# Performance work log

Hardware: AMD Instinct MI355X
Metric: run time of the kernel (lower is better)

Reference implementation:

```python
import jax, jax.numpy as jnp
import numpy as np

N_EMBD = 1024
N_HEAD = 16

def setup_inputs() -> dict:
    key = jax.random.key(0)
    ks = jax.random.split(key, 5)
    B, T, C = 4, 2048, N_EMBD
    x = jax.random.normal(ks[0], (B, T, C), dtype=jnp.float32)
    # torch nn.Linear weights: [out_features, in_features]
    w_attn = jax.random.normal(ks[1], (3 * C, C), dtype=jnp.float32) * (1.0 / np.sqrt(C))
    b_attn = jax.random.normal(ks[2], (3 * C,), dtype=jnp.float32) * 0.02
    w_proj = jax.random.normal(ks[3], (C, C), dtype=jnp.float32) * (1.0 / np.sqrt(C))
    b_proj = jax.random.normal(ks[4], (C,), dtype=jnp.float32) * 0.02
    return {"x": x, "w_attn": w_attn, "b_attn": b_attn, "w_proj": w_proj, "b_proj": b_proj}

def reference(x, w_attn, b_attn, w_proj, b_proj):
    B, T, C = x.shape
    H = N_HEAD
    D = C // H
    qkv = jnp.einsum('btc,oc->bto', x, w_attn) + b_attn  # [B,T,3C]
    q, k, v = jnp.split(qkv, 3, axis=-1)
    # [B,H,T,D]
    q = q.reshape(B, T, H, D).transpose(0, 2, 1, 3)
    k = k.reshape(B, T, H, D).transpose(0, 2, 1, 3)
    v = v.reshape(B, T, H, D).transpose(0, 2, 1, 3)
    att = jnp.einsum('bhqd,bhkd->bhqk', q, k) * (1.0 / np.sqrt(D))
    causal = jnp.tril(jnp.ones((T, T), dtype=bool))
    att = jnp.where(causal[None, None], att, -jnp.inf)
    att = jax.nn.softmax(att, axis=-1)
    y = jnp.einsum('bhqk,bhkd->bhqd', att, v)
    y = y.transpose(0, 2, 1, 3).reshape(B, T, C)
    return jnp.einsum('btc,oc->bto', y, w_proj) + b_proj
```

## Files before the change

kernel.cpp:

```cpp
#include <hip/hip_runtime.h>
#include <hip/hip_bf16.h>
#include <math.h>
#include <stdint.h>


typedef __attribute__((ext_vector_type(8))) short bf16x8;
typedef __attribute__((ext_vector_type(4))) float f32x4;

#define MFMA16(a, b, c) __builtin_amdgcn_mfma_f32_16x16x32_bf16((a), (b), (c), 0, 0, 0)

#define GLOAD_LDS16(gptr, lptr)                                                        \
  __builtin_amdgcn_global_load_lds((const __attribute__((address_space(1))) void*)(gptr), \
                                   (__attribute__((address_space(3))) void*)(lptr), 16, 0, 0)

__device__ __forceinline__ short f2bf(float f) {
  uint32_t u = __builtin_bit_cast(uint32_t, f);
  u = (u + 0x7FFFu + ((u >> 16) & 1u)) >> 16;
  return (short)u;
}

__device__ __forceinline__ uint32_t cvtpk_bf16(float a, float b) {
  uint32_t pk;
  asm("v_cvt_pk_bf16_f32 %0, %1, %2" : "=v"(pk) : "v"(a), "v"(b));
  return pk;
}

__global__ void cvt3_f32_bf16(const float* __restrict__ x, short* __restrict__ ox, int nx4,
                              const float* __restrict__ wa, short* __restrict__ owa, int nwa4,
                              const float* __restrict__ wp, short* __restrict__ owp, int nwp4) {
  int i = blockIdx.x * 256 + threadIdx.x;
  const float* src;
  short* dst;
  int j;
  if (i < nx4) {
    src = x; dst = ox; j = i;
  } else if (i < nx4 + nwa4) {
    src = wa; dst = owa; j = i - nx4;
  } else if (i < nx4 + nwa4 + nwp4) {
    src = wp; dst = owp; j = i - nx4 - nwa4;
  } else {
    return;
  }
  float4 v = ((const float4*)src)[j];
  short4 o;
  o.x = f2bf(v.x); o.y = f2bf(v.y); o.z = f2bf(v.z); o.w = f2bf(v.w);
  ((short4*)dst)[j] = o;
}

template <int MODE>
__global__ __launch_bounds__(256, 3)
void gemm_bt(const short* __restrict__ A, const short* __restrict__ B,
             const float* __restrict__ bias, int K, int N,
             short* __restrict__ q, short* __restrict__ kk,
             short* __restrict__ vt, float* __restrict__ out) {
  __shared__ short As[128 * 32];
  __shared__ short Bs[128 * 32];
  const int tid = threadIdx.x;
  const int lane = tid & 63;
  const int w = tid >> 6;
  const int wm = w >> 1, wn = w & 1;
  const int bn = blockIdx.x, bm = blockIdx.y;
  const char* Ab = (const char*)A + (size_t)bm * 128 * K * 2;
  const char* Bb = (const char*)B + (size_t)bn * 128 * K * 2;
  const int rstride = K * 2;

  f32x4 acc[4][4] = {};

  for (int k0 = 0; k0 < K; k0 += 32) {
#pragma unroll
    for (int i = 0; i < 2; ++i) {
      const int off = i * 4096 + w * 1024 + lane * 16;
      const int row = off >> 6, cb = off & 63;
      GLOAD_LDS16(Ab + (size_t)row * rstride + k0 * 2 + cb, (char*)As + off);
      GLOAD_LDS16(Bb + (size_t)row * rstride + k0 * 2 + cb, (char*)Bs + off);
    }
    __syncthreads();

    bf16x8 a[4], b[4];
#pragma unroll
    for (int mi = 0; mi < 4; ++mi)
      a[mi] = *(const bf16x8*)&As[(wm * 64 + mi * 16 + (lane & 15)) * 32 + (lane >> 4) * 8];
#pragma unroll
    for (int ni = 0; ni < 4; ++ni)
      b[ni] = *(const bf16x8*)&Bs[(wn * 64 + ni * 16 + (lane & 15)) * 32 + (lane >> 4) * 8];
#pragma unroll
    for (int mi = 0; mi < 4; ++mi)
#pragma unroll
      for (int ni = 0; ni < 4; ++ni)
        acc[mi][ni] = MFMA16(a[mi], b[ni], acc[mi][ni]);
    __syncthreads();
  }

  if (MODE == 0) {
    const int part = bn >> 3;
    if (part == 2) {
      const int bb = bm >> 4;
#pragma unroll
      for (int mi = 0; mi < 4; ++mi) {
        const int t0 = (bm & 15) * 128 + wm * 64 + mi * 16 + (lane >> 4) * 4;
#pragma unroll
        for (int ni = 0; ni < 4; ++ni) {
          const int c = bn * 128 + wn * 64 + ni * 16 + (lane & 15) - 2048;
          const int h = c >> 6, d = c & 63;
          const float bv = bias[c + 2048];
          uint2 pk;
          pk.x = cvtpk_bf16(acc[mi][ni][0] + bv, acc[mi][ni][1] + bv);
          pk.y = cvtpk_bf16(acc[mi][ni][2] + bv, acc[mi][ni][3] + bv);
          *(uint2*)&vt[(((size_t)bb * 16 + h) * 64 + d) * 2048 + t0] = pk;
        }
      }
    } else {
      short* dst = (part == 0) ? q : kk;
      const float sc = (part == 0) ? 0.125f * 1.44269504f : 1.0f;
#pragma unroll
      for (int mi = 0; mi < 4; ++mi) {
#pragma unroll
        for (int ni = 0; ni < 4; ++ni) {
          const int n = bn * 128 + wn * 64 + ni * 16 + (lane & 15);
          const int c = n & 1023, h = c >> 6, d = c & 63;
          const float bv = bias[n];
#pragma unroll
          for (int r = 0; r < 4; ++r) {
            const int m = bm * 128 + wm * 64 + mi * 16 + (lane >> 4) * 4 + r;
            const int bb = m >> 11, t = m & 2047;
            dst[(((size_t)bb * 16 + h) * 2048 + t) * 64 + d] =
                f2bf((acc[mi][ni][r] + bv) * sc);
          }
        }
      }
    }
  } else {
#pragma unroll
    for (int mi = 0; mi < 4; ++mi)
#pragma unroll
      for (int ni = 0; ni < 4; ++ni) {
        const int n = bn * 128 + wn * 64 + ni * 16 + (lane & 15);
        const float bv = bias[n];
#pragma unroll
        for (int r = 0; r < 4; ++r) {
          const int m = bm * 128 + wm * 64 + mi * 16 + (lane >> 4) * 4 + r;
          out[(size_t)m * N + n] = acc[mi][ni][r] + bv;
        }
      }
  }
}

__global__ __launch_bounds__(256, 3)
void attn64(const short* __restrict__ Q, const short* __restrict__ Kd,
            const short* __restrict__ Vt, short* __restrict__ Y) {
  const int o = blockIdx.x;
  const int swz = (o & 7) * 256 + (o >> 3);
  const int bh = swz >> 5;
  const int qb = 31 - (swz & 31);
  const int tid = threadIdx.x, lane = tid & 63, w = tid >> 6;

  __shared__ short Ks[2][64 * 64];
  __shared__ short Vs[2][64 * 64];
  __shared__ short Ps[4][16 * 64];

  const char* qg = (const char*)(Q + (size_t)bh * 2048 * 64);
  const char* kg = (const char*)(Kd + (size_t)bh * 2048 * 64);
  const char* vg = (const char*)(Vt + (size_t)bh * 64 * 2048);

  bf16x8 qa[2];
  const int qrowA = qb * 64 + w * 16 + (lane & 15);
#pragma unroll
  for (int dc = 0; dc < 2; ++dc)
    qa[dc] = *(const bf16x8*)(qg + (size_t)qrowA * 128 + dc * 64 + (lane >> 4) * 16);

  bf16x8 bones;
  {
    const short v = ((lane & 15) == 0) ? (short)0x3F80 : (short)0;
#pragma unroll
    for (int j = 0; j < 8; ++j) bones[j] = v;
  }

  auto stage = [&](int buf, int kt) {
#pragma unroll
    for (int i = 0; i < 2; ++i) {
      const int off = i * 4096 + w * 1024 + lane * 16;
      const int row = off >> 7, cb = off & 127;
      const int scb = cb ^ ((row & 7) << 4);
      GLOAD_LDS16(kg + (size_t)(kt * 64 + row) * 128 + scb, (char*)Ks[buf] + off);
      GLOAD_LDS16(vg + (size_t)row * 4096 + kt * 128 + scb, (char*)Vs[buf] + off);
    }
  };

  f32x4 oacc[4] = {};
  f32x4 lacc = {};
  const int qrowD = qb * 64 + w * 16 + (lane >> 4) * 4;

  stage(0, 0);
  __syncthreads();
  int cur = 0;

  for (int kt = 0; kt <= qb; ++kt) {
    if (kt < qb) stage(cur ^ 1, kt + 1);

    const char* ks = (const char*)Ks[cur];
    const char* vs = (const char*)Vs[cur];

    f32x4 sacc[4] = {};
    __builtin_amdgcn_s_setprio(1);
#pragma unroll
    for (int dc = 0; dc < 2; ++dc) {
#pragma unroll
      for (int ni = 0; ni < 4; ++ni) {
        const int row = ni * 16 + (lane & 15);
        const int bo = (dc * 64 + (lane >> 4) * 16) ^ ((row & 7) << 4);
        bf16x8 kf = *(const bf16x8*)(ks + row * 128 + bo);
        sacc[ni] = MFMA16(qa[dc], kf, sacc[ni]);
      }
    }
    __builtin_amdgcn_s_setprio(0);

    if (kt == qb) {
#pragma unroll
      for (int ni = 0; ni < 4; ++ni) {
        const int col = kt * 64 + ni * 16 + (lane & 15);
#pragma unroll
        for (int r = 0; r < 4; ++r)
          if (col > qrowD + r) sacc[ni][r] = -INFINITY;
      }
    }

#pragma unroll
    for (int r = 0; r < 4; ++r)
#pragma unroll
      for (int ni = 0; ni < 4; ++ni)
        sacc[ni][r] = exp2f(sacc[ni][r]);

    char* pw = (char*)&Ps[w][0];
#pragma unroll
    for (int r = 0; r < 4; ++r) {
      const int prow = (lane >> 4) * 4 + r;
      const int rowoff = prow * 128;
      const int sw = (prow & 7) << 4;
#pragma unroll
      for (int ni = 0; ni < 4; ni += 2) {
        const uint32_t pk = cvtpk_bf16(sacc[ni][r], sacc[ni + 1][r]);
        const int a0 = rowoff + ((((ni) * 16 + (lane & 15)) * 2) ^ sw);
        const int a1 = rowoff + ((((ni + 1) * 16 + (lane & 15)) * 2) ^ sw);
        *(short*)(pw + a0) = (short)(pk & 0xFFFFu);
        *(short*)(pw + a1) = (short)(pk >> 16);
      }
    }
    asm volatile("s_waitcnt lgkmcnt(0)" ::: "memory");

    bf16x8 pa[2];
#pragma unroll
    for (int kc = 0; kc < 2; ++kc) {
      const int prow = lane & 15;
      const int pbo = (kc * 64 + (lane >> 4) * 16) ^ ((prow & 7) << 4);
      pa[kc] = *(const bf16x8*)(pw + prow * 128 + pbo);
    }

    __builtin_amdgcn_s_setprio(1);
#pragma unroll
    for (int nd = 0; nd < 4; ++nd)
#pragma unroll
      for (int kc = 0; kc < 2; ++kc) {
        const int row = nd * 16 + (lane & 15);
        const int bo = (kc * 64 + (lane >> 4) * 16) ^ ((row & 7) << 4);
        bf16x8 vf = *(const bf16x8*)(vs + row * 128 + bo);
        oacc[nd] = MFMA16(pa[kc], vf, oacc[nd]);
      }
    lacc = MFMA16(pa[0], bones, lacc);
    lacc = MFMA16(pa[1], bones, lacc);
    __builtin_amdgcn_s_setprio(0);

    __syncthreads();
    cur ^= 1;
  }

  float linv[4];
#pragma unroll
  for (int r = 0; r < 4; ++r) {
    const float l = __shfl(lacc[r], lane & 48);
    linv[r] = 1.0f / l;
  }

  char* pw = (char*)&Ps[w][0];
  const int qloc0 = (lane >> 4) * 4;
#pragma unroll
  for (int nd = 0; nd < 4; ++nd)
#pragma unroll
    for (int r = 0; r < 4; ++r) {
      const int row = qloc0 + r;
      const int bo = (nd * 32 + (lane & 15) * 2) ^ ((row & 7) << 4);
      *(short*)(pw + row * 128 + bo) = f2bf(oacc[nd][r] * linv[r]);
    }
  asm volatile("s_waitcnt lgkmcnt(0)" ::: "memory");

  const int b = bh >> 4, h = bh & 15;
#pragma unroll
  for (int half = 0; half < 2; ++half) {
    const int qlocal = half * 8 + (lane >> 3);
    const int dstart = (lane & 7) * 8;
    const int bo = (dstart * 2) ^ ((qlocal & 7) << 4);
    bf16x8 v = *(const bf16x8*)(pw + qlocal * 128 + bo);
    const int t = qb * 64 + w * 16 + qlocal;
    *(bf16x8*)&Y[((size_t)b * 2048 + t) * 1024 + h * 64 + dstart] = v;
  }
}

extern "C" void kernel_launch(void* const* d_in, const int* in_sizes, int n_in,
                              void* d_out, int out_size, void* d_ws, size_t ws_size,
                              hipStream_t stream) {
  const float* x = (const float*)d_in[0];
  const float* w_attn = (const float*)d_in[1];
  const float* b_attn = (const float*)d_in[2];
  const float* w_proj = (const float*)d_in[3];
  const float* b_proj = (const float*)d_in[4];
  float* out = (float*)d_out;

  char* ws = (char*)d_ws;
  size_t o = 0;
  const size_t SZ = (size_t)8192 * 1024 * 2;
  short* xb = (short*)(ws + o);  o += SZ;
  short* wab = (short*)(ws + o); o += (size_t)3072 * 1024 * 2;
  short* wpb = (short*)(ws + o); o += (size_t)1024 * 1024 * 2;
  short* qw = (short*)(ws + o);  o += SZ;
  short* kw = (short*)(ws + o);  o += SZ;
  short* vtw = (short*)(ws + o); o += SZ;
  short* yb = xb;

  cvt3_f32_bf16<<<12288, 256, 0, stream>>>(x, xb, 2097152,
                                           w_attn, wab, 786432,
                                           w_proj, wpb, 262144);

  gemm_bt<0><<<dim3(24, 64), 256, 0, stream>>>(xb, wab, b_attn, 1024, 3072,
                                               qw, kw, vtw, nullptr);
  attn64<<<2048, 256, 0, stream>>>(qw, kw, vtw, yb);
  gemm_bt<1><<<dim3(8, 64), 256, 0, stream>>>(yb, wpb, b_proj, 1024, 1024,
                                              nullptr, nullptr, nullptr, out);
}
```

Measured before the change: 282.0 us.

## Process two 64-row query sub-tiles per attention block to reuse K/V tiles

Each attention block now handles 128 query rows as two 64-row sub-tiles. It loads each K/V tile into LDS once and uses it for both sub-tiles, and the grid is halved to 1024 blocks. This is meant to halve K/V global loads and staging per query row and to amortise barriers. It raises register pressure because Q fragments and accumulators are doubled, it makes the causal workload per block coarser, and launch bounds are changed to target 4 blocks per CU.

```diff
diff --git a/kernel.cpp b/kernel.cpp
--- a/kernel.cpp
+++ b/kernel.cpp
@@ -145,13 +145,13 @@
   }
 }
 
-__global__ __launch_bounds__(256, 3)
+__global__ __launch_bounds__(256, 4)
 void attn64(const short* __restrict__ Q, const short* __restrict__ Kd,
             const short* __restrict__ Vt, short* __restrict__ Y) {
   const int o = blockIdx.x;
-  const int swz = (o & 7) * 256 + (o >> 3);
-  const int bh = swz >> 5;
-  const int qb = 31 - (swz & 31);
+  const int swz = (o & 7) * 128 + (o >> 3);
+  const int bh = swz >> 4;
+  const int qb = 15 - (swz & 15);
   const int tid = threadIdx.x, lane = tid & 63, w = tid >> 6;
 
   __shared__ short Ks[2][64 * 64];
@@ -162,11 +162,14 @@
   const char* kg = (const char*)(Kd + (size_t)bh * 2048 * 64);
   const char* vg = (const char*)(Vt + (size_t)bh * 64 * 2048);
 
-  bf16x8 qa[2];
-  const int qrowA = qb * 64 + w * 16 + (lane & 15);
-#pragma unroll
-  for (int dc = 0; dc < 2; ++dc)
-    qa[dc] = *(const bf16x8*)(qg + (size_t)qrowA * 128 + dc * 64 + (lane >> 4) * 16);
+  bf16x8 qa[2][2];
+#pragma unroll
+  for (int s = 0; s < 2; ++s) {
+    const int qrowA = qb * 128 + s * 64 + w * 16 + (lane & 15);
+#pragma unroll
+    for (int dc = 0; dc < 2; ++dc)
+      qa[s][dc] = *(const bf16x8*)(qg + (size_t)qrowA * 128 + dc * 64 + (lane >> 4) * 16);
+  }
 
   bf16x8 bones;
   {
@@ -186,121 +189,130 @@
     }
   };
 
-  f32x4 oacc[4] = {};
-  f32x4 lacc = {};
-  const int qrowD = qb * 64 + w * 16 + (lane >> 4) * 4;
+  f32x4 oacc[2][4] = {};
+  f32x4 lacc[2] = {};
+  const int ktmax = 2 * qb + 1;
 
   stage(0, 0);
   __syncthreads();
   int cur = 0;
 
-  for (int kt = 0; kt <= qb; ++kt) {
-    if (kt < qb) stage(cur ^ 1, kt + 1);
+  for (int kt = 0; kt <= ktmax; ++kt) {
+    if (kt < ktmax) stage(cur ^ 1, kt + 1);
 
     const char* ks = (const char*)Ks[cur];
     const char* vs = (const char*)Vs[cur];
-
-    f32x4 sacc[4] = {};
-    __builtin_amdgcn_s_setprio(1);
-#pragma unroll
-    for (int dc = 0; dc < 2; ++dc) {
-#pragma unroll
-      for (int ni = 0; ni < 4; ++ni) {
-        const int row = ni * 16 + (lane & 15);
-        const int bo = (dc * 64 + (lane >> 4) * 16) ^ ((row & 7) << 4);
-        bf16x8 kf = *(const bf16x8*)(ks + row * 128 + bo);
-        sacc[ni] = MFMA16(qa[dc], kf, sacc[ni]);
-      }
-    }
-    __builtin_amdgcn_s_setprio(0);
-
-    if (kt == qb) {
-#pragma unroll
-      for (int ni = 0; ni < 4; ++ni) {
-        const int col = kt * 64 + ni * 16 + (lane & 15);
-#pragma unroll
-        for (int r = 0; r < 4; ++r)
-          if (col > qrowD + r) sacc[ni][r] = -INFINITY;
-      }
-    }
-
-#pragma unroll
-    for (int r = 0; r < 4; ++r)
-#pragma unroll
-      for (int ni = 0; ni < 4; ++ni)
-        sacc[ni][r] = exp2f(sacc[ni][r]);
-
     char* pw = (char*)&Ps[w][0];
-#pragma unroll
-    for (int r = 0; r < 4; ++r) {
-      const int prow = (lane >> 4) * 4 + r;
-      const int rowoff = prow * 128;
-      const int sw = (prow & 7) << 4;
-#pragma unroll
-      for (int ni = 0; ni < 4; ni += 2) {
-        const uint32_t pk = cvtpk_bf16(sacc[ni][r], sacc[ni + 1][r]);
-        const int a0 = rowoff + ((((ni) * 16 + (lane & 15)) * 2) ^ sw);
-        const int a1 = rowoff + ((((ni + 1) * 16 + (lane & 15)) * 2) ^ sw);
-        *(short*)(pw + a0) = (short)(pk & 0xFFFFu);
-        *(short*)(pw + a1) = (short)(pk >> 16);
-      }
-    }
-    asm volatile("s_waitcnt lgkmcnt(0)" ::: "memory");
-
-    bf16x8 pa[2];
-#pragma unroll
-    for (int kc = 0; kc < 2; ++kc) {
-      const int prow = lane & 15;
-      const int pbo = (kc * 64 + (lane >> 4) * 16) ^ ((prow & 7) << 4);
-      pa[kc] = *(const bf16x8*)(pw + prow * 128 + pbo);
-    }
-
-    __builtin_amdgcn_s_setprio(1);
-#pragma unroll
-    for (int nd = 0; nd < 4; ++nd)
+
+#pragma unroll
+    for (int s = 0; s < 2; ++s) {
+      if (s == 0 && kt == ktmax) continue;
+
+      f32x4 sacc[4] = {};
+      __builtin_amdgcn_s_setprio(1);
+#pragma unroll
+      for (int dc = 0; dc < 2; ++dc) {
+#pragma unroll
+        for (int ni = 0; ni < 4; ++ni) {
+          const int row = ni * 16 + (lane & 15);
+          const int bo = (dc * 64 + (lane >> 4) * 16) ^ ((row & 7) << 4);
+          bf16x8 kf = *(const bf16x8*)(ks + row * 128 + bo);
+          sacc[ni] = MFMA16(qa[s][dc], kf, sacc[ni]);
+        }
+      }
+      __builtin_amdgcn_s_setprio(0);
+
+      if (kt == 2 * qb + s) {
+        const int qrowD = qb * 128 + s * 64 + w * 16 + (lane >> 4) * 4;
+#pragma unroll
+        for (int ni = 0; ni < 4; ++ni) {
+          const int col = kt * 64 + ni * 16 + (lane & 15);
+#pragma unroll
+          for (int r = 0; r < 4; ++r)
+            if (col > qrowD + r) sacc[ni][r] = -INFINITY;
+        }
+      }
+
+#pragma unroll
+      for (int r = 0; r < 4; ++r)
+#pragma unroll
+        for (int ni = 0; ni < 4; ++ni)
+          sacc[ni][r] = exp2f(sacc[ni][r]);
+
+#pragma unroll
+      for (int r = 0; r < 4; ++r) {
+        const int prow = (lane >> 4) * 4 + r;
+        const int rowoff = prow * 128;
+        const int sw = (prow & 7) << 4;
+#pragma unroll
+        for (int ni = 0; ni < 4; ni += 2) {
+          const uint32_t pk = cvtpk_bf16(sacc[ni][r], sacc[ni + 1][r]);
+          const int a0 = rowoff + ((((ni) * 16 + (lane & 15)) * 2) ^ sw);
+          const int a1 = rowoff + ((((ni + 1) * 16 + (lane & 15)) * 2) ^ sw);
+          *(short*)(pw + a0) = (short)(pk & 0xFFFFu);
+          *(short*)(pw + a1) = (short)(pk >> 16);
+        }
+      }
+      asm volatile("s_waitcnt lgkmcnt(0)" ::: "memory");
+
+      bf16x8 pa[2];
 #pragma unroll
       for (int kc = 0; kc < 2; ++kc) {
-        const int row = nd * 16 + (lane & 15);
-        const int bo = (kc * 64 + (lane >> 4) * 16) ^ ((row & 7) << 4);
-        bf16x8 vf = *(const bf16x8*)(vs + row * 128 + bo);
-        oacc[nd] = MFMA16(pa[kc], vf, oacc[nd]);
-      }
-    lacc = MFMA16(pa[0], bones, lacc);
-    lacc = MFMA16(pa[1], bones, lacc);
-    __builtin_amdgcn_s_setprio(0);
+        const int prow = lane & 15;
+        const int pbo = (kc * 64 + (lane >> 4) * 16) ^ ((prow & 7) << 4);
+        pa[kc] = *(const bf16x8*)(pw + prow * 128 + pbo);
+      }
+
+      __builtin_amdgcn_s_setprio(1);
+#pragma unroll
+      for (int nd = 0; nd < 4; ++nd)
+#pragma unroll
+        for (int kc = 0; kc < 2; ++kc) {
+          const int row = nd * 16 + (lane & 15);
+          const int bo = (kc * 64 + (lane >> 4) * 16) ^ ((row & 7) << 4);
+          bf16x8 vf = *(const bf16x8*)(vs + row * 128 + bo);
+          oacc[s][nd] = MFMA16(pa[kc], vf, oacc[s][nd]);
+        }
+      lacc[s] = MFMA16(pa[0], bones, lacc[s]);
+      lacc[s] = MFMA16(pa[1], bones, lacc[s]);
+      __builtin_amdgcn_s_setprio(0);
+    }
 
     __syncthreads();
     cur ^= 1;
   }
 
-  float linv[4];
-#pragma unroll
-  for (int r = 0; r < 4; ++r) {
-    const float l = __shfl(lacc[r], lane & 48);
-    linv[r] = 1.0f / l;
-  }
-
+  const int b = bh >> 4, h = bh & 15;
   char* pw = (char*)&Ps[w][0];
   const int qloc0 = (lane >> 4) * 4;
 #pragma unroll
-  for (int nd = 0; nd < 4; ++nd)
+  for (int s = 0; s < 2; ++s) {
+    float linv[4];
 #pragma unroll
     for (int r = 0; r < 4; ++r) {
-      const int row = qloc0 + r;
-      const int bo = (nd * 32 + (lane & 15) * 2) ^ ((row & 7) << 4);
-      *(short*)(pw + row * 128 + bo) = f2bf(oacc[nd][r] * linv[r]);
-    }
-  asm volatile("s_waitcnt lgkmcnt(0)" ::: "memory");
-
-  const int b = bh >> 4, h = bh & 15;
-#pragma unroll
-  for (int half = 0; half < 2; ++half) {
-    const int qlocal = half * 8 + (lane >> 3);
-    const int dstart = (lane & 7) * 8;
-    const int bo = (dstart * 2) ^ ((qlocal & 7) << 4);
-    bf16x8 v = *(const bf16x8*)(pw + qlocal * 128 + bo);
-    const int t = qb * 64 + w * 16 + qlocal;
-    *(bf16x8*)&Y[((size_t)b * 2048 + t) * 1024 + h * 64 + dstart] = v;
+      const float l = __shfl(lacc[s][r], lane & 48);
+      linv[r] = 1.0f / l;
+    }
+#pragma unroll
+    for (int nd = 0; nd < 4; ++nd)
+#pragma unroll
+      for (int r = 0; r < 4; ++r) {
+        const int row = qloc0 + r;
+        const int bo = (nd * 32 + (lane & 15) * 2) ^ ((row & 7) << 4);
+        *(short*)(pw + row * 128 + bo) = f2bf(oacc[s][nd][r] * linv[r]);
+      }
+    asm volatile("s_waitcnt lgkmcnt(0)" ::: "memory");
+
+#pragma unroll
+    for (int half = 0; half < 2; ++half) {
+      const int qlocal = half * 8 + (lane >> 3);
+      const int dstart = (lane & 7) * 8;
+      const int bo = (dstart * 2) ^ ((qlocal & 7) << 4);
+      bf16x8 v = *(const bf16x8*)(pw + qlocal * 128 + bo);
+      const int t = qb * 128 + s * 64 + w * 16 + qlocal;
+      *(bf16x8*)&Y[((size_t)b * 2048 + t) * 1024 + h * 64 + dstart] = v;
+    }
+    asm volatile("s_waitcnt lgkmcnt(0)" ::: "memory");
   }
 }
 
@@ -331,7 +343,7 @@
 
   gemm_bt<0><<<dim3(24, 64), 256, 0, stream>>>(xb, wab, b_attn, 1024, 3072,
                                                qw, kw, vtw, nullptr);
-  attn64<<<2048, 256, 0, stream>>>(qw, kw, vtw, yb);
+  attn64<<<1024, 256, 0, stream>>>(qw, kw, vtw, yb);
   gemm_bt<1><<<dim3(8, 64), 256, 0, stream>>>(yb, wpb, b_proj, 1024, 1024,
                                               nullptr, nullptr, nullptr, out);
 }
```

New measurement: 300.6 us. +6.6%, slower.

## Load K and V fragments directly from global memory instead of LDS staging

Applied to the files above, without the earlier changes.

Removes the double-buffered LDS staging of K and V tiles and the per-iteration block barrier in the attention kernel. Each wave now reads its K and V MFMA fragments straight from global memory, relying on L1/L2 caching since all four waves read the same tiles. This frees LDS and raises the occupancy hint from 3 to 6 blocks per CU, at the cost of redundant global loads per wave and less latency hiding.

```diff
diff --git a/kernel.cpp b/kernel.cpp
--- a/kernel.cpp
+++ b/kernel.cpp
@@ -145,7 +145,7 @@
   }
 }
 
-__global__ __launch_bounds__(256, 3)
+__global__ __launch_bounds__(256, 6)
 void attn64(const short* __restrict__ Q, const short* __restrict__ Kd,
             const short* __restrict__ Vt, short* __restrict__ Y) {
   const int o = blockIdx.x;
@@ -154,8 +154,6 @@
   const int qb = 31 - (swz & 31);
   const int tid = threadIdx.x, lane = tid & 63, w = tid >> 6;
 
-  __shared__ short Ks[2][64 * 64];
-  __shared__ short Vs[2][64 * 64];
   __shared__ short Ps[4][16 * 64];
 
   const char* qg = (const char*)(Q + (size_t)bh * 2048 * 64);
@@ -175,40 +173,20 @@
     for (int j = 0; j < 8; ++j) bones[j] = v;
   }
 
-  auto stage = [&](int buf, int kt) {
-#pragma unroll
-    for (int i = 0; i < 2; ++i) {
-      const int off = i * 4096 + w * 1024 + lane * 16;
-      const int row = off >> 7, cb = off & 127;
-      const int scb = cb ^ ((row & 7) << 4);
-      GLOAD_LDS16(kg + (size_t)(kt * 64 + row) * 128 + scb, (char*)Ks[buf] + off);
-      GLOAD_LDS16(vg + (size_t)row * 4096 + kt * 128 + scb, (char*)Vs[buf] + off);
-    }
-  };
-
   f32x4 oacc[4] = {};
   f32x4 lacc = {};
   const int qrowD = qb * 64 + w * 16 + (lane >> 4) * 4;
-
-  stage(0, 0);
-  __syncthreads();
-  int cur = 0;
+  char* pw = (char*)&Ps[w][0];
 
   for (int kt = 0; kt <= qb; ++kt) {
-    if (kt < qb) stage(cur ^ 1, kt + 1);
-
-    const char* ks = (const char*)Ks[cur];
-    const char* vs = (const char*)Vs[cur];
-
     f32x4 sacc[4] = {};
     __builtin_amdgcn_s_setprio(1);
 #pragma unroll
     for (int dc = 0; dc < 2; ++dc) {
 #pragma unroll
       for (int ni = 0; ni < 4; ++ni) {
-        const int row = ni * 16 + (lane & 15);
-        const int bo = (dc * 64 + (lane >> 4) * 16) ^ ((row & 7) << 4);
-        bf16x8 kf = *(const bf16x8*)(ks + row * 128 + bo);
+        const int row = kt * 64 + ni * 16 + (lane & 15);
+        bf16x8 kf = *(const bf16x8*)(kg + (size_t)row * 128 + dc * 64 + (lane >> 4) * 16);
         sacc[ni] = MFMA16(qa[dc], kf, sacc[ni]);
       }
     }
@@ -230,7 +208,6 @@
       for (int ni = 0; ni < 4; ++ni)
         sacc[ni][r] = exp2f(sacc[ni][r]);
 
-    char* pw = (char*)&Ps[w][0];
 #pragma unroll
     for (int r = 0; r < 4; ++r) {
       const int prow = (lane >> 4) * 4 + r;
@@ -261,16 +238,13 @@
 #pragma unroll
       for (int kc = 0; kc < 2; ++kc) {
         const int row = nd * 16 + (lane & 15);
-        const int bo = (kc * 64 + (lane >> 4) * 16) ^ ((row & 7) << 4);
-        bf16x8 vf = *(const bf16x8*)(vs + row * 128 + bo);
+        bf16x8 vf = *(const bf16x8*)(vg + (size_t)row * 4096 + kt * 128 +
+                                     kc * 64 + (lane >> 4) * 16);
         oacc[nd] = MFMA16(pa[kc], vf, oacc[nd]);
       }
     lacc = MFMA16(pa[0], bones, lacc);
     lacc = MFMA16(pa[1], bones, lacc);
     __builtin_amdgcn_s_setprio(0);
-
-    __syncthreads();
-    cur ^= 1;
   }
 
   float linv[4];
@@ -280,7 +254,6 @@
     linv[r] = 1.0f / l;
   }
 
-  char* pw = (char*)&Ps[w][0];
   const int qloc0 = (lane >> 4) * 4;
 #pragma unroll
   for (int nd = 0; nd < 4; ++nd)
```

Result: slower. 560.0 us (+98.6%).
